# Kernel tuning notes

Hardware: AMD Instinct MI355X
Metric: run time of the kernel (lower is better)

The kernel has to match this reference:

```python
import jax, jax.numpy as jnp
import numpy as np

B, S, D, H = 4, 2048, 1024, 16
DK = D // H

def setup_inputs() -> dict:
    key = jax.random.key(0)
    ks = jax.random.split(key, 8)
    q = jax.random.normal(ks[0], (B, S, D), dtype=jnp.float32)
    k = jax.random.normal(ks[1], (B, S, D), dtype=jnp.float32)
    v = jax.random.normal(ks[2], (B, S, D), dtype=jnp.float32)
    # broadcastable causal mask [1,1,S,S]; 0 -> masked
    mask = jnp.tril(jnp.ones((S, S), dtype=jnp.int32))[None, None]
    sc = 1.0 / np.sqrt(D)
    w_q = jax.random.normal(ks[3], (D, D), dtype=jnp.float32) * sc
    w_k = jax.random.normal(ks[4], (D, D), dtype=jnp.float32) * sc
    w_v = jax.random.normal(ks[5], (D, D), dtype=jnp.float32) * sc
    w_o = jax.random.normal(ks[6], (D, D), dtype=jnp.float32) * sc
    return {"q": q, "k": k, "v": v, "mask": mask,
            "w_q": w_q, "w_k": w_k, "w_v": w_v, "w_o": w_o}


def reference(q, k, v, mask, w_q, w_k, w_v, w_o):
    # Linear (no bias): x @ W^T, torch convention
    def proj(x, w):
        return jnp.einsum('bsd,ed->bse', x, w)
    # [B,S,D] -> [B,H,S,DK]
    def split_heads(x):
        return x.reshape(B, S, H, DK).transpose(0, 2, 1, 3)

    query = split_heads(proj(q, w_q))
    key_ = split_heads(proj(k, w_k))
    value = split_heads(proj(v, w_v))

    scores = jnp.einsum('bhqd,bhkd->bhqk', query, key_) / jnp.sqrt(
        jnp.asarray(DK, dtype=query.dtype))
    scores = jnp.where(mask == 0, jnp.asarray(-1e9, dtype=scores.dtype), scores)
    attn = jax.nn.softmax(scores, axis=-1)  # dropout p=0.0 -> identity
    x = jnp.einsum('bhqk,bhkd->bhqd', attn, value)
    x = x.transpose(0, 2, 1, 3).reshape(B, S, D)
    return jnp.einsum('bsd,ed->bse', x, w_o)
```

## Files before the change

### kernel.cpp

```cpp
#include <hip/hip_runtime.h>
#include <hip/hip_bf16.h>

#define B_ 4
#define S_ 2048
#define D_ 1024
#define H_ 16
#define DK_ 64

typedef unsigned short u16;
typedef __bf16 bf16x8 __attribute__((ext_vector_type(8)));
typedef float f32x4 __attribute__((ext_vector_type(4)));

typedef const unsigned int __attribute__((address_space(1))) guint;
typedef unsigned int __attribute__((address_space(3))) luint;

__device__ __forceinline__ void gld16(const u16* g, u16* l) {
  __builtin_amdgcn_global_load_lds((guint*)g, (luint*)l, 16, 0, 0);
}

__device__ __forceinline__ u16 f2b(float f) {
  __hip_bfloat16 h = __float2bfloat16(f);
  return __builtin_bit_cast(u16, h);
}
__device__ __forceinline__ ushort4 f2b4(float4 f) {
  ushort4 r;
  r.x = f2b(f.x); r.y = f2b(f.y); r.z = f2b(f.z); r.w = f2b(f.w);
  return r;
}
__device__ __forceinline__ bf16x8 ldb8(const u16* p) {
  union { uint4 u; bf16x8 v; } x;
  x.u = *(const uint4*)p;
  return x.v;
}

struct CvtAllArgs {
  const float* s[7];
  u16* d[7];
};
__global__ __launch_bounds__(256) void cvt_all(CvtAllArgs a) {
  const int z = blockIdx.y;
  const int bx = blockIdx.x;
  const float* s;
  u16* d;
  int i;
  if (z < 3) {
    s = a.s[z]; d = a.d[z];
    i = bx * 256 + threadIdx.x;
  } else {
    if (bx >= 2048) return;
    const int wsel = bx >> 9;
    s = a.s[3 + wsel]; d = a.d[3 + wsel];
    i = (bx & 511) * 256 + threadIdx.x;
  }
  float4 x = ((const float4*)s)[2 * i];
  float4 y = ((const float4*)s)[2 * i + 1];
  ((ushort4*)d)[2 * i] = f2b4(x);
  ((ushort4*)d)[2 * i + 1] = f2b4(y);
}

__device__ __forceinline__ void swz_bnbm(int& bn, int& bm) {
  const int id2 = blockIdx.y * 8 + blockIdx.x;
  const int wg = (id2 & 7) * 64 + (id2 >> 3);
  bn = wg & 7;
  bm = wg >> 3;
}

template <bool OUT_QKV>
__device__ __forceinline__ void gemm_body(const u16* __restrict__ A,
                                          const u16* __restrict__ W,
                                          void* __restrict__ C, float scale) {
  constexpr int K = D_;
  __shared__ u16 As[128 * 32];
  __shared__ u16 Ws[128 * 32];
  const int t = threadIdx.x;
  const int lane = t & 63, w = t >> 6;
  const int quad = lane >> 4, m16 = lane & 15;
  int bn, bm;
  swz_bnbm(bn, bm);
  const int wm = (w >> 1) * 64, wn = (w & 1) * 64;
  const int sr = lane >> 2, sc8 = (lane & 3) * 8;

  f32x4 acc[4][4];
  const f32x4 zero = {0.f, 0.f, 0.f, 0.f};
#pragma unroll
  for (int i = 0; i < 4; i++)
#pragma unroll
    for (int j = 0; j < 4; j++) acc[i][j] = zero;

  const u16* Ag = A + (size_t)(bm * 128 + w * 32 + sr) * K + sc8;
  const u16* Wg = W + (size_t)(bn * 128 + w * 32 + sr) * K + sc8;
  u16* AsB = &As[w * 1024];
  u16* WsB = &Ws[w * 1024];

  for (int k0 = 0; k0 < K; k0 += 32) {
    __syncthreads();
    gld16(Ag + k0, AsB);
    gld16(Ag + (size_t)16 * K + k0, AsB + 512);
    gld16(Wg + k0, WsB);
    gld16(Wg + (size_t)16 * K + k0, WsB + 512);
    __syncthreads();

    bf16x8 af[4], wf[4];
#pragma unroll
    for (int mt = 0; mt < 4; mt++)
      af[mt] = ldb8(&As[(wm + mt * 16 + m16) * 32 + quad * 8]);
#pragma unroll
    for (int nt = 0; nt < 4; nt++)
      wf[nt] = ldb8(&Ws[(wn + nt * 16 + m16) * 32 + quad * 8]);
#pragma unroll
    for (int mt = 0; mt < 4; mt++)
#pragma unroll
      for (int nt = 0; nt < 4; nt++)
        acc[mt][nt] = __builtin_amdgcn_mfma_f32_16x16x32_bf16(af[mt], wf[nt],
                                                              acc[mt][nt], 0, 0, 0);
  }

#pragma unroll
  for (int mt = 0; mt < 4; mt++) {
#pragma unroll
    for (int r = 0; r < 4; r++) {
      int m = bm * 128 + wm + mt * 16 + quad * 4 + r;
#pragma unroll
      for (int nt = 0; nt < 4; nt++) {
        int n = bn * 128 + wn + nt * 16 + m16;
        float val = acc[mt][nt][r] * scale;
        if (OUT_QKV) {
          int b = m >> 11, s = m & (S_ - 1);
          int h = n >> 6, dk = n & 63;
          ((u16*)C)[(((size_t)b * H_ + h) * S_ + s) * DK_ + dk] = f2b(val);
        } else {
          ((float*)C)[(size_t)m * D_ + n] = val;
        }
      }
    }
  }
}

struct GemmQkvArgs {
  const u16 *a0, *a1, *a2;
  const u16 *w0, *w1, *w2;
  u16 *c0, *c1, *c2;
  float qscale;
};
__global__ __launch_bounds__(256) void gemm_qkv(GemmQkvArgs g) {
  const int z = blockIdx.z;
  const u16* A = z == 0 ? g.a0 : z == 1 ? g.a1 : g.a2;
  const u16* W = z == 0 ? g.w0 : z == 1 ? g.w1 : g.w2;
  u16* C = z == 0 ? g.c0 : z == 1 ? g.c1 : g.c2;
  gemm_body<true>(A, W, C, z == 0 ? g.qscale : 1.0f);
}

__global__ __launch_bounds__(256) void gemm_o(const u16* __restrict__ A,
                                              const u16* __restrict__ W,
                                              float* __restrict__ C) {
  gemm_body<false>(A, W, C, 1.0f);
}

__global__ __launch_bounds__(256) void transpose_v(const u16* __restrict__ Vp,
                                                   u16* __restrict__ VpT) {
  constexpr int LDT = 72;
  __shared__ u16 T[64 * LDT];
  const int t = threadIdx.x;
  const int s0 = blockIdx.x * 64, bh = blockIdx.y;
  const size_t base = (size_t)bh * S_ * DK_;
  const int rot = t & 7;
#pragma unroll
  for (int i = 0; i < 2; i++) {
    int c = t + i * 256, row = c >> 3, c8 = (c & 7) * 8;
    union { uint4 u; u16 s[8]; } uv;
    uv.u = *(const uint4*)(Vp + base + (size_t)(s0 + row) * DK_ + c8);
#pragma unroll
    for (int j0 = 0; j0 < 8; j0++) {
      int j = (j0 + rot) & 7;
      T[(c8 + j) * LDT + row] = uv.s[j];
    }
  }
  __syncthreads();
#pragma unroll
  for (int i = 0; i < 2; i++) {
    int c = t + i * 256, row = c >> 3, c8 = (c & 7) * 8;
    uint4 val = *(const uint4*)&T[row * LDT + c8];
    *(uint4*)(VpT + base + (size_t)row * S_ + s0 + c8) = val;
  }
}

__global__ __launch_bounds__(512, 4) void flash_attn(const u16* __restrict__ Qp,
                                                     const u16* __restrict__ Kp,
                                                     const u16* __restrict__ VpT,
                                                     u16* __restrict__ Xb) {
  constexpr int LDK = 72;
  __shared__ u16 Ks[2][64 * LDK];
  __shared__ u16 Vt[2][64 * LDK];
  __shared__ u16 Ps[8][16 * LDK];
  const int t = threadIdx.x;
  const int lane = t & 63, w = t >> 6;
  const int quad = lane >> 4, m16 = lane & 15;
  const int id = blockIdx.x;
  const int g = (id >> 3) & 7;
  const int bh = (id & 7) * 8 + (id >> 6);
  const int b = bh >> 4, h = bh & (H_ - 1);
  const size_t base = (size_t)bh * S_ * DK_;
  const int srow = t >> 3, sc8 = (t & 7) * 8;
  const f32x4 zero = {0.f, 0.f, 0.f, 0.f};

#pragma unroll 1
  for (int pi = 0; pi < 2; pi++) {
    const int qt = pi ? (15 - g) : g;
    const int q0 = qt * 128;
    const int nT = 2 * qt + 2;

    const int qrow = q0 + w * 16 + m16;
    bf16x8 qf0 = ldb8(Qp + base + (size_t)qrow * DK_ + quad * 8);
    bf16x8 qf1 = ldb8(Qp + base + (size_t)qrow * DK_ + 32 + quad * 8);

    f32x4 acc[4];
#pragma unroll
    for (int i = 0; i < 4; i++) acc[i] = zero;
    float rsum[4] = {0.f, 0.f, 0.f, 0.f};

    uint4 kr = *(const uint4*)(Kp + base + (size_t)srow * DK_ + sc8);
    uint4 vr = *(const uint4*)(VpT + base + (size_t)srow * S_ + sc8);

#pragma unroll 1
    for (int ti = 0; ti < nT; ti++) {
      const int kt0 = ti * 64;
      const int cur = ti & 1;
      *(uint4*)&Ks[cur][srow * LDK + sc8] = kr;
      *(uint4*)&Vt[cur][srow * LDK + sc8] = vr;
      __syncthreads();
      if (ti + 1 < nT) {
        kr = *(const uint4*)(Kp + base + (size_t)(kt0 + 64 + srow) * DK_ + sc8);
        vr = *(const uint4*)(VpT + base + (size_t)srow * S_ + kt0 + 64 + sc8);
      }
      const u16* Kc = Ks[cur];
      const u16* Vc = Vt[cur];

      f32x4 sc[4];
      __builtin_amdgcn_s_setprio(1);
#pragma unroll
      for (int nt = 0; nt < 4; nt++) {
        bf16x8 kf0 = ldb8(&Kc[(nt * 16 + m16) * LDK + quad * 8]);
        bf16x8 kf1 = ldb8(&Kc[(nt * 16 + m16) * LDK + 32 + quad * 8]);
        sc[nt] = __builtin_amdgcn_mfma_f32_16x16x32_bf16(kf0, qf0, zero, 0, 0, 0);
        sc[nt] = __builtin_amdgcn_mfma_f32_16x16x32_bf16(kf1, qf1, sc[nt], 0, 0, 0);
      }
      __builtin_amdgcn_s_setprio(0);

      if (ti >= nT - 2) {
        const int qcol = q0 + w * 16 + m16;
#pragma unroll
        for (int nt = 0; nt < 4; nt++) {
          int kg = kt0 + nt * 16 + quad * 4;
#pragma unroll
          for (int r = 0; r < 4; r++)
            if (kg + r > qcol) sc[nt][r] = -1e30f;
        }
      }

      u16* Pw = &Ps[w][0];
#pragma unroll
      for (int nt = 0; nt < 4; nt++) {
        ushort4 pk;
        float p0 = __builtin_amdgcn_exp2f(sc[nt][0]);
        float p1 = __builtin_amdgcn_exp2f(sc[nt][1]);
        float p2 = __builtin_amdgcn_exp2f(sc[nt][2]);
        float p3 = __builtin_amdgcn_exp2f(sc[nt][3]);
        rsum[nt] += (p0 + p1) + (p2 + p3);
        pk.x = f2b(p0); pk.y = f2b(p1); pk.z = f2b(p2); pk.w = f2b(p3);
        *(ushort4*)&Pw[m16 * LDK + nt * 16 + quad * 4] = pk;
      }

      __builtin_amdgcn_s_setprio(1);
#pragma unroll
      for (int s2 = 0; s2 < 2; s2++) {
        bf16x8 pf = ldb8(&Pw[m16 * LDK + s2 * 32 + quad * 8]);
#pragma unroll
        for (int nt = 0; nt < 4; nt++) {
          bf16x8 vf = ldb8(&Vc[(nt * 16 + m16) * LDK + s2 * 32 + quad * 8]);
          acc[nt] = __builtin_amdgcn_mfma_f32_16x16x32_bf16(pf, vf, acc[nt], 0, 0, 0);
        }
      }
      __builtin_amdgcn_s_setprio(0);
    }

    float tot = (rsum[0] + rsum[1]) + (rsum[2] + rsum[3]);
    tot += __shfl_xor(tot, 16);
    tot += __shfl_xor(tot, 32);
    float rcv[4];
#pragma unroll
    for (int r = 0; r < 4; r++)
      rcv[r] = __builtin_amdgcn_rcpf(__shfl(tot, quad * 4 + r, 16));
#pragma unroll
    for (int nt = 0; nt < 4; nt++)
#pragma unroll
      for (int r = 0; r < 4; r++) {
        int rg = q0 + w * 16 + quad * 4 + r;
        Xb[((size_t)b * S_ + rg) * D_ + h * DK_ + nt * 16 + m16] =
            f2b(acc[nt][r] * rcv[r]);
      }
  }
}

extern "C" void kernel_launch(void* const* d_in, const int* in_sizes, int n_in,
                              void* d_out, int out_size, void* d_ws, size_t ws_size,
                              hipStream_t stream) {
  (void)in_sizes; (void)n_in; (void)out_size; (void)ws_size;
  const float* q = (const float*)d_in[0];
  const float* k = (const float*)d_in[1];
  const float* v = (const float*)d_in[2];
  const float* wq = (const float*)d_in[4];
  const float* wk = (const float*)d_in[5];
  const float* wv = (const float*)d_in[6];
  const float* wo = (const float*)d_in[7];

  const size_t nBSD = (size_t)B_ * S_ * D_;
  const size_t nDD = (size_t)D_ * D_;
  u16* ab = (u16*)d_ws;
  u16* wqb = ab + nBSD;
  u16* wkb = wqb + nDD;
  u16* wvb = wkb + nDD;
  u16* wob = wvb + nDD;
  u16* Qp = wob + nDD;
  u16* Kp = Qp + nBSD;
  u16* Vp = Kp + nBSD;
  u16* VpT = ab;
  u16* Xb = Vp;
  u16* abk = (u16*)d_out;
  u16* abv = abk + nBSD;

  const float qscale = 0.125f * 1.44269504089f;

  CvtAllArgs ca = {{q, k, v, wq, wk, wv, wo}, {ab, abk, abv, wqb, wkb, wvb, wob}};
  cvt_all<<<dim3(nBSD / 2048, 4), 256, 0, stream>>>(ca);

  GemmQkvArgs gq = {ab, abk, abv, wqb, wkb, wvb, Qp, Kp, Vp, qscale};
  gemm_qkv<<<dim3(D_ / 128, (B_ * S_) / 128, 3), 256, 0, stream>>>(gq);

  transpose_v<<<dim3(S_ / 64, B_ * H_), 256, 0, stream>>>(Vp, VpT);
  flash_attn<<<512, 512, 0, stream>>>(Qp, Kp, VpT, Xb);

  gemm_o<<<dim3(D_ / 128, (B_ * S_) / 128), 256, 0, stream>>>(Xb, wob, (float*)d_out);
}
```

Baseline: 326.8 us.

## Rewrite projection GEMMs with 128x256 tiles, triple-buffered LDS and swizzle

```diff
diff --git a/kernel.cpp b/kernel.cpp
--- a/kernel.cpp
+++ b/kernel.cpp
@@ -58,27 +58,36 @@
   ((ushort4*)d)[2 * i + 1] = f2b4(y);
 }
 
-__device__ __forceinline__ void swz_bnbm(int& bn, int& bm) {
-  const int id2 = blockIdx.y * 8 + blockIdx.x;
-  const int wg = (id2 & 7) * 64 + (id2 >> 3);
-  bn = wg & 7;
-  bm = wg >> 3;
-}
-
 template <bool OUT_QKV>
-__device__ __forceinline__ void gemm_body(const u16* __restrict__ A,
-                                          const u16* __restrict__ W,
-                                          void* __restrict__ C, float scale) {
+__device__ __forceinline__ void gemm_body2(const u16* __restrict__ A,
+                                           const u16* __restrict__ W,
+                                           void* __restrict__ C, float scale,
+                                           int bm, int bn) {
   constexpr int K = D_;
-  __shared__ u16 As[128 * 32];
-  __shared__ u16 Ws[128 * 32];
+  constexpr int NS = K / 32;
+  __shared__ u16 Ab[3 * 4096];
+  __shared__ u16 Bb[3 * 8192];
   const int t = threadIdx.x;
   const int lane = t & 63, w = t >> 6;
   const int quad = lane >> 4, m16 = lane & 15;
-  int bn, bm;
-  swz_bnbm(bn, bm);
-  const int wm = (w >> 1) * 64, wn = (w & 1) * 64;
-  const int sr = lane >> 2, sc8 = (lane & 3) * 8;
+  const int wm = w >> 2, wn = w & 3;
+
+  int aoff[4], boff[4];
+#pragma unroll
+  for (int i = 0; i < 4; i++) {
+    int a = (wm * 64 + i * 16 + m16) * 64 + quad * 16;
+    a ^= ((a >> 7) & 3) << 4;
+    aoff[i] = a >> 1;
+    int bb = (wn * 64 + i * 16 + m16) * 64 + quad * 16;
+    bb ^= ((bb >> 7) & 3) << 4;
+    boff[i] = bb >> 1;
+  }
+
+  const int cs8 = ((t & 3) ^ ((t >> 3) & 3)) * 8;
+  const u16* aps = A + (size_t)(bm * 128 + (t >> 2)) * K + cs8;
+  const u16* bps0 = W + (size_t)(bn * 256 + (t >> 2)) * K + cs8;
+  const u16* bps1 = W + (size_t)(bn * 256 + 128 + (t >> 2)) * K + cs8;
+  const int wb = w * 512;
 
   f32x4 acc[4][4];
   const f32x4 zero = {0.f, 0.f, 0.f, 0.f};
@@ -87,43 +96,75 @@
 #pragma unroll
     for (int j = 0; j < 4; j++) acc[i][j] = zero;
 
-  const u16* Ag = A + (size_t)(bm * 128 + w * 32 + sr) * K + sc8;
-  const u16* Wg = W + (size_t)(bn * 128 + w * 32 + sr) * K + sc8;
-  u16* AsB = &As[w * 1024];
-  u16* WsB = &Ws[w * 1024];
-
-  for (int k0 = 0; k0 < K; k0 += 32) {
-    __syncthreads();
-    gld16(Ag + k0, AsB);
-    gld16(Ag + (size_t)16 * K + k0, AsB + 512);
-    gld16(Wg + k0, WsB);
-    gld16(Wg + (size_t)16 * K + k0, WsB + 512);
-    __syncthreads();
-
-    bf16x8 af[4], wf[4];
-#pragma unroll
-    for (int mt = 0; mt < 4; mt++)
-      af[mt] = ldb8(&As[(wm + mt * 16 + m16) * 32 + quad * 8]);
-#pragma unroll
-    for (int nt = 0; nt < 4; nt++)
-      wf[nt] = ldb8(&Ws[(wn + nt * 16 + m16) * 32 + quad * 8]);
-#pragma unroll
-    for (int mt = 0; mt < 4; mt++)
-#pragma unroll
-      for (int nt = 0; nt < 4; nt++)
-        acc[mt][nt] = __builtin_amdgcn_mfma_f32_16x16x32_bf16(af[mt], wf[nt],
-                                                              acc[mt][nt], 0, 0, 0);
-  }
-
-#pragma unroll
-  for (int mt = 0; mt < 4; mt++) {
+  gld16(aps, &Ab[wb]);
+  gld16(bps0, &Bb[wb]);
+  gld16(bps1, &Bb[4096 + wb]);
+  gld16(aps + 32, &Ab[4096 + wb]);
+  gld16(bps0 + 32, &Bb[8192 + wb]);
+  gld16(bps1 + 32, &Bb[8192 + 4096 + wb]);
+  aps += 64; bps0 += 64; bps1 += 64;
+  asm volatile("s_waitcnt vmcnt(3)" ::: "memory");
+  __builtin_amdgcn_s_barrier();
+  __builtin_amdgcn_sched_barrier(0);
+
+  int cb = 0, nb = 1, sb = 2;
+#pragma unroll 1
+  for (int s = 0; s < NS; s++) {
+    const u16* Ac = &Ab[cb * 4096];
+    const u16* Bc = &Bb[cb * 8192];
+    const bool st = (s + 2 < NS);
+    if (st) gld16(aps, &Ab[sb * 4096 + wb]);
+    bf16x8 bf0 = ldb8(Bc + boff[0]);
+    bf16x8 bf1 = ldb8(Bc + boff[1]);
+    bf16x8 bf2 = ldb8(Bc + boff[2]);
+    bf16x8 bf3 = ldb8(Bc + boff[3]);
+    bf16x8 a0 = ldb8(Ac + aoff[0]);
+    bf16x8 a1 = ldb8(Ac + aoff[1]);
+    __builtin_amdgcn_s_setprio(1);
+    acc[0][0] = __builtin_amdgcn_mfma_f32_16x16x32_bf16(a0, bf0, acc[0][0], 0, 0, 0);
+    acc[0][1] = __builtin_amdgcn_mfma_f32_16x16x32_bf16(a0, bf1, acc[0][1], 0, 0, 0);
+    acc[0][2] = __builtin_amdgcn_mfma_f32_16x16x32_bf16(a0, bf2, acc[0][2], 0, 0, 0);
+    acc[0][3] = __builtin_amdgcn_mfma_f32_16x16x32_bf16(a0, bf3, acc[0][3], 0, 0, 0);
+    acc[1][0] = __builtin_amdgcn_mfma_f32_16x16x32_bf16(a1, bf0, acc[1][0], 0, 0, 0);
+    acc[1][1] = __builtin_amdgcn_mfma_f32_16x16x32_bf16(a1, bf1, acc[1][1], 0, 0, 0);
+    acc[1][2] = __builtin_amdgcn_mfma_f32_16x16x32_bf16(a1, bf2, acc[1][2], 0, 0, 0);
+    acc[1][3] = __builtin_amdgcn_mfma_f32_16x16x32_bf16(a1, bf3, acc[1][3], 0, 0, 0);
+    __builtin_amdgcn_s_setprio(0);
+    __builtin_amdgcn_s_barrier();
+    if (st) {
+      gld16(bps0, &Bb[sb * 8192 + wb]);
+      gld16(bps1, &Bb[sb * 8192 + 4096 + wb]);
+    }
+    bf16x8 a2 = ldb8(Ac + aoff[2]);
+    bf16x8 a3 = ldb8(Ac + aoff[3]);
+    __builtin_amdgcn_s_setprio(1);
+    acc[2][0] = __builtin_amdgcn_mfma_f32_16x16x32_bf16(a2, bf0, acc[2][0], 0, 0, 0);
+    acc[2][1] = __builtin_amdgcn_mfma_f32_16x16x32_bf16(a2, bf1, acc[2][1], 0, 0, 0);
+    acc[2][2] = __builtin_amdgcn_mfma_f32_16x16x32_bf16(a2, bf2, acc[2][2], 0, 0, 0);
+    acc[2][3] = __builtin_amdgcn_mfma_f32_16x16x32_bf16(a2, bf3, acc[2][3], 0, 0, 0);
+    acc[3][0] = __builtin_amdgcn_mfma_f32_16x16x32_bf16(a3, bf0, acc[3][0], 0, 0, 0);
+    acc[3][1] = __builtin_amdgcn_mfma_f32_16x16x32_bf16(a3, bf1, acc[3][1], 0, 0, 0);
+    acc[3][2] = __builtin_amdgcn_mfma_f32_16x16x32_bf16(a3, bf2, acc[3][2], 0, 0, 0);
+    acc[3][3] = __builtin_amdgcn_mfma_f32_16x16x32_bf16(a3, bf3, acc[3][3], 0, 0, 0);
+    __builtin_amdgcn_s_setprio(0);
+    if (st) asm volatile("s_waitcnt vmcnt(3)" ::: "memory");
+    else    asm volatile("s_waitcnt vmcnt(0)" ::: "memory");
+    __builtin_amdgcn_sched_barrier(0);
+    __builtin_amdgcn_s_barrier();
+    __builtin_amdgcn_sched_barrier(0);
+    aps += 32; bps0 += 32; bps1 += 32;
+    int tmp = cb; cb = nb; nb = sb; sb = tmp;
+  }
+
+#pragma unroll
+  for (int mi = 0; mi < 4; mi++) {
 #pragma unroll
     for (int r = 0; r < 4; r++) {
-      int m = bm * 128 + wm + mt * 16 + quad * 4 + r;
-#pragma unroll
-      for (int nt = 0; nt < 4; nt++) {
-        int n = bn * 128 + wn + nt * 16 + m16;
-        float val = acc[mt][nt][r] * scale;
+      int m = bm * 128 + wm * 64 + mi * 16 + quad * 4 + r;
+#pragma unroll
+      for (int nf = 0; nf < 4; nf++) {
+        int n = bn * 256 + wn * 64 + nf * 16 + m16;
+        float val = acc[mi][nf][r] * scale;
         if (OUT_QKV) {
           int b = m >> 11, s = m & (S_ - 1);
           int h = n >> 6, dk = n & 63;
@@ -142,18 +183,24 @@
   u16 *c0, *c1, *c2;
   float qscale;
 };
-__global__ __launch_bounds__(256) void gemm_qkv(GemmQkvArgs g) {
-  const int z = blockIdx.z;
-  const u16* A = z == 0 ? g.a0 : z == 1 ? g.a1 : g.a2;
-  const u16* W = z == 0 ? g.w0 : z == 1 ? g.w1 : g.w2;
-  u16* C = z == 0 ? g.c0 : z == 1 ? g.c1 : g.c2;
-  gemm_body<true>(A, W, C, z == 0 ? g.qscale : 1.0f);
-}
-
-__global__ __launch_bounds__(256) void gemm_o(const u16* __restrict__ A,
-                                              const u16* __restrict__ W,
-                                              float* __restrict__ C) {
-  gemm_body<false>(A, W, C, 1.0f);
+__global__ __launch_bounds__(512, 2) void gemm_qkv(GemmQkvArgs g) {
+  const int id3 = (blockIdx.z * 64 + blockIdx.y) * 4 + blockIdx.x;
+  const int wgn = (id3 & 7) * 96 + (id3 >> 3);
+  const int zz = wgn >> 8, rem = wgn & 255;
+  const int bm = rem >> 2, bn = rem & 3;
+  const u16* A = zz == 0 ? g.a0 : zz == 1 ? g.a1 : g.a2;
+  const u16* W = zz == 0 ? g.w0 : zz == 1 ? g.w1 : g.w2;
+  u16* C = zz == 0 ? g.c0 : zz == 1 ? g.c1 : g.c2;
+  gemm_body2<true>(A, W, C, zz == 0 ? g.qscale : 1.0f, bm, bn);
+}
+
+__global__ __launch_bounds__(512, 2) void gemm_o(const u16* __restrict__ A,
+                                                 const u16* __restrict__ W,
+                                                 float* __restrict__ C) {
+  const int id2 = blockIdx.y * 4 + blockIdx.x;
+  const int wgn = (id2 & 7) * 32 + (id2 >> 3);
+  const int bm = wgn >> 2, bn = wgn & 3;
+  gemm_body2<false>(A, W, C, 1.0f, bm, bn);
 }
 
 __global__ __launch_bounds__(256) void transpose_v(const u16* __restrict__ Vp,
@@ -334,10 +381,10 @@
   cvt_all<<<dim3(nBSD / 2048, 4), 256, 0, stream>>>(ca);
 
   GemmQkvArgs gq = {ab, abk, abv, wqb, wkb, wvb, Qp, Kp, Vp, qscale};
-  gemm_qkv<<<dim3(D_ / 128, (B_ * S_) / 128, 3), 256, 0, stream>>>(gq);
+  gemm_qkv<<<dim3(4, 64, 3), 512, 0, stream>>>(gq);
 
   transpose_v<<<dim3(S_ / 64, B_ * H_), 256, 0, stream>>>(Vp, VpT);
   flash_attn<<<512, 512, 0, stream>>>(Qp, Kp, VpT, Xb);
 
-  gemm_o<<<dim3(D_ / 128, (B_ * S_) / 128), 256, 0, stream>>>(Xb, wob, (float*)d_out);
-}
+  gemm_o<<<dim3(4, 64), 512, 0, stream>>>(Xb, wob, (float*)d_out);
+}
```

Measured after the change: 327.1 us. No clear change (+0.1%).
